# Kernel optimization log

Measured on AMD Instinct MI355X. Metric: run time of the kernel, lower is better.

## Reference

```python
import jax, jax.numpy as jnp
import numpy as np

N_WIRES = 8
DIM = 2 ** N_WIRES  # 256
NUM_HEADS = 4

def _cnot_ring_perm():
    # Compose CNOT(w, w+1) for w=0..6 then CNOT(7, 0) into one basis permutation.
    # Wire 0 is the most-significant bit of the basis index.
    perm = np.arange(DIM)
    pairs = [(w, w + 1) for w in range(N_WIRES - 1)] + [(N_WIRES - 1, 0)]
    j = np.arange(DIM)
    for c, t in pairs:
        ctrl = (j >> (N_WIRES - 1 - c)) & 1
        M = j ^ (ctrl << (N_WIRES - 1 - t))  # flip target bit where control=1 (involution)
        perm = perm[M]
    return perm

PERM = _cnot_ring_perm()
# SIGNS[i, w] = <i|Z_w|i> = 1 - 2*bit_w(i)
SIGNS = np.array([[1.0 - 2.0 * ((i >> (N_WIRES - 1 - w)) & 1) for w in range(N_WIRES)]
                  for i in range(DIM)], dtype=np.float32)

def setup_inputs() -> dict:
    key = jax.random.key(0)
    k1, k2, k3 = jax.random.split(key, 3)
    x = jax.random.normal(k1, (16, 4096, N_WIRES), jnp.float32)  # rotation angles per token
    theta = jax.random.normal(k2, (N_WIRES,), jnp.float32)       # trainable RX params
    w_combine = jax.random.normal(k3, (N_WIRES, N_WIRES), jnp.float32) / np.float32(np.sqrt(N_WIRES))
    b_combine = jnp.zeros((N_WIRES,), jnp.float32)
    return {"x": x, "theta": theta, "w_combine": w_combine, "b_combine": b_combine}

def _quantum_features(x, theta):
    # RX(x_i) then RX(theta_i) on wire i compose to RX(x_i + theta_i) acting on |0>.
    B, S, E = x.shape
    N = B * S
    phi = (x + theta).reshape(N, E)
    c = jnp.cos(0.5 * phi).astype(jnp.complex64)
    s = (-1j) * jnp.sin(0.5 * phi)          # RX|0> = cos(phi/2)|0> - i sin(phi/2)|1>
    wv = jnp.stack([c, s.astype(jnp.complex64)], axis=-1)  # (N, 8, 2)
    # Build product state via successive Kronecker products (wire 0 = MSB).
    state = jnp.ones((N, 1), jnp.complex64)
    for w in range(E):
        state = (state[:, :, None] * wv[:, w, None, :]).reshape(N, -1)  # (N, 2^(w+1))
    state = state[:, jnp.asarray(PERM)]      # apply the CNOT ring as one permutation
    probs = state.real ** 2 + state.imag ** 2  # (N, 256)
    return (probs @ jnp.asarray(SIGNS)).reshape(B, S, E)  # <Z_w> per token

def reference(x, theta, w_combine, b_combine):
    B, S, E = x.shape
    d_k = E // NUM_HEADS
    q = _quantum_features(x, theta)           # (B, S, 8); k = v = q in the source
    scores = jnp.einsum('bse,bte->bst', q, q) / np.float32(np.sqrt(d_k))
    attn = jax.nn.softmax(scores, axis=-1)    # dropout is identity in eval mode
    out = jnp.einsum('bst,bte->bse', attn, q)
    # Faithful to source: transpose(1,2).contiguous().view(B, S, E)
    out = jnp.swapaxes(out, 1, 2).reshape(B, S, E)
    return out @ w_combine.T + b_combine
```

## Files before the change

kernel.cpp:

```cpp
#include <hip/hip_runtime.h>
#include <math.h>


#define SEQ   4096
#define NB    16
#define SROWS 128
#define TPB   1024
#define NTG   4
#define TC    1024
#define TILES_PER_TG 8
#define KSTR  12

typedef _Float16 f16x4  __attribute__((ext_vector_type(4)));
typedef float    f32x16 __attribute__((ext_vector_type(16)));

#if __has_builtin(__builtin_amdgcn_exp2f)
#define EXP2F(x) __builtin_amdgcn_exp2f(x)
#else
#define EXP2F(x) exp2f(x)
#endif

__global__ __launch_bounds__(TPB, 8)
void qattn_kernel(const float* __restrict__ x, const float* __restrict__ theta,
                  const float* __restrict__ wc, const float* __restrict__ bc,
                  float* __restrict__ out)
{
    __shared__ __align__(16) _Float16 kf[TC * KSTR];
    __shared__ __align__(16) _Float16 vt[10 * TC];
    float* part = (float*)kf;
    float* attn = (float*)vt;

    const int tid  = threadIdx.x;
    const int lane = tid & 63;
    const int wv   = tid >> 6;
    const int sub  = wv & 3;
    const int tg   = wv >> 2;
    const int l31  = lane & 31;
    const int hp   = lane >> 5;

    const int b  = blockIdx.x >> 5;
    const int S0 = (blockIdx.x & 31) * SROWS;
    const float* xb = x + (size_t)b * SEQ * 8;

    float th[8];
#pragma unroll
    for (int w = 0; w < 8; ++w) th[w] = theta[w];

    f16x4 qfrag;
    {
        const int s = S0 + sub * 32 + l31;
        const float4 xa  = *(const float4*)(xb + s * 8);
        const float4 xb4 = *(const float4*)(xb + s * 8 + 4);
        float c0 = __cosf(xa.x  + th[0]);
        float c1 = __cosf(xa.y  + th[1]);
        float c2 = __cosf(xa.z  + th[2]);
        float c3 = __cosf(xa.w  + th[3]);
        float c4 = __cosf(xb4.x + th[4]);
        float c5 = __cosf(xb4.y + th[5]);
        float c6 = __cosf(xb4.z + th[6]);
        float c7 = __cosf(xb4.w + th[7]);
        float p1 = c0 * c1, p2 = p1 * c2, p3 = p2 * c3, p4 = p3 * c4;
        float p5 = p4 * c5, p6 = p5 * c6, p7 = p6 * c7;
        float p0 = c1 * c2 * c3 * c4 * c5 * c6 * c7;
        const float sc = 0.70710678118654752f * 1.44269504088896341f;
        if (hp == 0)
            qfrag = (f16x4){(_Float16)(p0*sc), (_Float16)(p1*sc),
                            (_Float16)(p2*sc), (_Float16)(p3*sc)};
        else
            qfrag = (f16x4){(_Float16)(p4*sc), (_Float16)(p5*sc),
                            (_Float16)(p6*sc), (_Float16)(p7*sc)};
    }

    f32x16 o = {0.f,0.f,0.f,0.f,0.f,0.f,0.f,0.f,0.f,0.f,0.f,0.f,0.f,0.f,0.f,0.f};

    const int wr = (l31 < 9) ? l31 : 9;
    const int vx = 2 * wr;
    const _Float16* kfb = kf + l31 * KSTR + 4 * hp + (tg * TILES_PER_TG) * 32 * KSTR;

    for (int ch = 0; ch < SEQ / TC; ++ch) {
        __syncthreads();
        {
            const int tt = tid;
            const int t  = ch * TC + tt;
            const float4 xa  = *(const float4*)(xb + t * 8);
            const float4 xb4 = *(const float4*)(xb + t * 8 + 4);
            float c0 = __cosf(xa.x  + th[0]);
            float c1 = __cosf(xa.y  + th[1]);
            float c2 = __cosf(xa.z  + th[2]);
            float c3 = __cosf(xa.w  + th[3]);
            float c4 = __cosf(xb4.x + th[4]);
            float c5 = __cosf(xb4.y + th[5]);
            float c6 = __cosf(xb4.z + th[6]);
            float c7 = __cosf(xb4.w + th[7]);
            float p1 = c0 * c1, p2 = p1 * c2, p3 = p2 * c3, p4 = p3 * c4;
            float p5 = p4 * c5, p6 = p5 * c6, p7 = p6 * c7;
            float p0 = c1 * c2 * c3 * c4 * c5 * c6 * c7;
            _Float16 h0 = (_Float16)p0, h1 = (_Float16)p1, h2 = (_Float16)p2,
                     h3 = (_Float16)p3, h4 = (_Float16)p4, h5 = (_Float16)p5,
                     h6 = (_Float16)p6, h7 = (_Float16)p7;
            _Float16* krow = kf + tt * KSTR;
            *(f16x4*)(krow)     = (f16x4){h0, h1, h2, h3};
            *(f16x4*)(krow + 4) = (f16x4){h4, h5, h6, h7};
            const int c  = tt >> 1;
            const int hb = tt & 1;
            vt[2*(0*512 + (c ^  0)) + hb] = h0;
            vt[2*(1*512 + (c ^  2)) + hb] = h1;
            vt[2*(2*512 + (c ^  4)) + hb] = h2;
            vt[2*(3*512 + (c ^  6)) + hb] = h3;
            vt[2*(4*512 + (c ^  8)) + hb] = h4;
            vt[2*(5*512 + (c ^ 10)) + hb] = h5;
            vt[2*(6*512 + (c ^ 12)) + hb] = h6;
            vt[2*(7*512 + (c ^ 14)) + hb] = h7;
            vt[2*(8*512 + (c ^ 16)) + hb] = (_Float16)1.0f;
        }
        __syncthreads();
#pragma unroll 2
        for (int i = 0; i < TILES_PER_TG; ++i) {
            f16x4 kfrag = *(const f16x4*)(kfb + i * 32 * KSTR);
            f32x16 cc = __builtin_amdgcn_mfma_f32_32x32x8f16(
                kfrag, qfrag, (f32x16){0.f,0.f,0.f,0.f,0.f,0.f,0.f,0.f,
                                       0.f,0.f,0.f,0.f,0.f,0.f,0.f,0.f}, 0, 0, 0);
#pragma unroll
            for (int u = 0; u < 4; ++u) {
                auto lo = __builtin_amdgcn_cvt_pkrtz(EXP2F(cc[4*u+0]), EXP2F(cc[4*u+1]));
                auto hi = __builtin_amdgcn_cvt_pkrtz(EXP2F(cc[4*u+2]), EXP2F(cc[4*u+3]));
                f16x4 pf;
                pf.x = lo.x; pf.y = lo.y; pf.z = hi.x; pf.w = hi.y;
                const int cw   = 16 * (tg * TILES_PER_TG + i) + 4*u + 2*hp;
                const int phys = wr * 512 + (cw ^ vx);
                f16x4 vfrag = *(const f16x4*)(vt + 2 * phys);
                o = __builtin_amdgcn_mfma_f32_32x32x8f16(pf, vfrag, o, 0, 0, 0);
            }
        }
    }

    __syncthreads();
    if (l31 < 9) {
#pragma unroll
        for (int r = 0; r < 16; ++r) {
            const int sloc = sub * 32 + (r & 3) + 8 * (r >> 2) + 4 * hp;
            part[((tg * SROWS) + sloc) * 9 + l31] = o[r];
        }
    }
    __syncthreads();
    for (int idx = tid; idx < SROWS * 9; idx += TPB) {
        const int rr = idx / 9;
        const int w  = idx - rr * 9;
        float sm = 0.f;
#pragma unroll
        for (int g = 0; g < NTG; ++g) sm += part[((g * SROWS) + rr) * 9 + w];
        attn[rr * 9 + w] = sm;
    }
    __syncthreads();
    if (tid < SROWS * 8) {
        const int rr = tid >> 3;
        const int w  = tid & 7;
        attn[rr * 9 + w] = attn[rr * 9 + w] / attn[rr * 9 + 8];
    }
    __syncthreads();

    if (tid < SROWS) {
        const int e    = tid >> 4;
        const int nloc = tid & 15;
        const int r    = e * 512 + (S0 >> 3) + nloc;
        float y[8];
#pragma unroll
        for (int c = 0; c < 8; ++c) y[c] = attn[(nloc * 8 + c) * 9 + e];
        float oo[8];
#pragma unroll
        for (int k = 0; k < 8; ++k) {
            float a = bc[k];
#pragma unroll
            for (int c = 0; c < 8; ++c) a += y[c] * wc[k * 8 + c];
            oo[k] = a;
        }
        float4* op = (float4*)(out + ((size_t)b * SEQ + r) * 8);
        op[0] = make_float4(oo[0], oo[1], oo[2], oo[3]);
        op[1] = make_float4(oo[4], oo[5], oo[6], oo[7]);
    }
}

extern "C" void kernel_launch(void* const* d_in, const int* in_sizes, int n_in,
                              void* d_out, int out_size, void* d_ws, size_t ws_size,
                              hipStream_t stream)
{
    const float* x  = (const float*)d_in[0];
    const float* th = (const float*)d_in[1];
    const float* wc = (const float*)d_in[2];
    const float* bc = (const float*)d_in[3];
    float* out = (float*)d_out;

    qattn_kernel<<<dim3(NB * (SEQ / SROWS)), dim3(TPB), 0, stream>>>(x, th, wc, bc, out);
}
```

Baseline: 96.40 us.

## Replace swizzled pairwise V layout with padded row-major V tile

Stores the value tile as nine padded rows of length 1028 halves instead of an XOR-swizzled pair-interleaved layout. Each thread now does plain contiguous writes and reads its f16x4 V fragment with a simple strided address. The padding is meant to spread rows across LDS banks, which removes the per-iteration XOR and index arithmetic. It also packs the exp results through a union and raises the inner-loop unroll from 2 to 4, which may raise register pressure.

```diff
diff --git a/kernel.cpp b/kernel.cpp
--- a/kernel.cpp
+++ b/kernel.cpp
@@ -10,9 +10,11 @@
 #define TC    1024
 #define TILES_PER_TG 8
 #define KSTR  12
+#define VSTR  1028
 
 typedef _Float16 f16x4  __attribute__((ext_vector_type(4)));
 typedef float    f32x16 __attribute__((ext_vector_type(16)));
+typedef __fp16   hf2    __attribute__((ext_vector_type(2)));
 
 #if __has_builtin(__builtin_amdgcn_exp2f)
 #define EXP2F(x) __builtin_amdgcn_exp2f(x)
@@ -26,7 +28,7 @@
                   float* __restrict__ out)
 {
     __shared__ __align__(16) _Float16 kf[TC * KSTR];
-    __shared__ __align__(16) _Float16 vt[10 * TC];
+    __shared__ __align__(16) _Float16 vt[9 * VSTR];
     float* part = (float*)kf;
     float* attn = (float*)vt;
 
@@ -73,9 +75,9 @@
 
     f32x16 o = {0.f,0.f,0.f,0.f,0.f,0.f,0.f,0.f,0.f,0.f,0.f,0.f,0.f,0.f,0.f,0.f};
 
-    const int wr = (l31 < 9) ? l31 : 9;
-    const int vx = 2 * wr;
+    const int wr = (l31 < 8) ? l31 : 8;
     const _Float16* kfb = kf + l31 * KSTR + 4 * hp + (tg * TILES_PER_TG) * 32 * KSTR;
+    const _Float16* vbb = vt + wr * VSTR + 4 * hp + tg * (TILES_PER_TG * 32);
 
     for (int ch = 0; ch < SEQ / TC; ++ch) {
         __syncthreads();
@@ -101,20 +103,18 @@
             _Float16* krow = kf + tt * KSTR;
             *(f16x4*)(krow)     = (f16x4){h0, h1, h2, h3};
             *(f16x4*)(krow + 4) = (f16x4){h4, h5, h6, h7};
-            const int c  = tt >> 1;
-            const int hb = tt & 1;
-            vt[2*(0*512 + (c ^  0)) + hb] = h0;
-            vt[2*(1*512 + (c ^  2)) + hb] = h1;
-            vt[2*(2*512 + (c ^  4)) + hb] = h2;
-            vt[2*(3*512 + (c ^  6)) + hb] = h3;
-            vt[2*(4*512 + (c ^  8)) + hb] = h4;
-            vt[2*(5*512 + (c ^ 10)) + hb] = h5;
-            vt[2*(6*512 + (c ^ 12)) + hb] = h6;
-            vt[2*(7*512 + (c ^ 14)) + hb] = h7;
-            vt[2*(8*512 + (c ^ 16)) + hb] = (_Float16)1.0f;
+            vt[0 * VSTR + tt] = h0;
+            vt[1 * VSTR + tt] = h1;
+            vt[2 * VSTR + tt] = h2;
+            vt[3 * VSTR + tt] = h3;
+            vt[4 * VSTR + tt] = h4;
+            vt[5 * VSTR + tt] = h5;
+            vt[6 * VSTR + tt] = h6;
+            vt[7 * VSTR + tt] = h7;
+            vt[8 * VSTR + tt] = (_Float16)1.0f;
         }
         __syncthreads();
-#pragma unroll 2
+#pragma unroll 4
         for (int i = 0; i < TILES_PER_TG; ++i) {
             f16x4 kfrag = *(const f16x4*)(kfb + i * 32 * KSTR);
             f32x16 cc = __builtin_amdgcn_mfma_f32_32x32x8f16(
@@ -122,14 +122,11 @@
                                        0.f,0.f,0.f,0.f,0.f,0.f,0.f,0.f}, 0, 0, 0);
 #pragma unroll
             for (int u = 0; u < 4; ++u) {
-                auto lo = __builtin_amdgcn_cvt_pkrtz(EXP2F(cc[4*u+0]), EXP2F(cc[4*u+1]));
-                auto hi = __builtin_amdgcn_cvt_pkrtz(EXP2F(cc[4*u+2]), EXP2F(cc[4*u+3]));
-                f16x4 pf;
-                pf.x = lo.x; pf.y = lo.y; pf.z = hi.x; pf.w = hi.y;
-                const int cw   = 16 * (tg * TILES_PER_TG + i) + 4*u + 2*hp;
-                const int phys = wr * 512 + (cw ^ vx);
-                f16x4 vfrag = *(const f16x4*)(vt + 2 * phys);
-                o = __builtin_amdgcn_mfma_f32_32x32x8f16(pf, vfrag, o, 0, 0, 0);
+                union { hf2 h[2]; f16x4 v; } pu;
+                pu.h[0] = __builtin_amdgcn_cvt_pkrtz(EXP2F(cc[4*u+0]), EXP2F(cc[4*u+1]));
+                pu.h[1] = __builtin_amdgcn_cvt_pkrtz(EXP2F(cc[4*u+2]), EXP2F(cc[4*u+3]));
+                f16x4 vfrag = *(const f16x4*)(vbb + i * 32 + u * 8);
+                o = __builtin_amdgcn_mfma_f32_32x32x8f16(pu.v, vfrag, o, 0, 0, 0);
             }
         }
     }
```

New measurement: 91.23 us. 5.4% less time.
